# Kernel optimization log

Measured on AMD Instinct MI355X. Metric: run time of the kernel, lower is better.

The kernel has to match this reference:

```python
import jax, jax.numpy as jnp
import numpy as np

HIDDEN = 512
NUM_HEADS = 8
PROJ = NUM_HEADS * HIDDEN  # 4096
B, N = 4, 2048
SCALE = (HIDDEN // NUM_HEADS) ** -0.5  # att_size ** -0.5 = 64 ** -0.5


def setup_inputs() -> dict:
    key = jax.random.key(0)
    ks = jax.random.split(key, 11)
    init = lambda k, shape, fan_in: jax.random.normal(k, shape, jnp.float32) * (fan_in ** -0.5)
    return {
        "q": jax.random.normal(ks[0], (B, N, HIDDEN), jnp.float32),
        "k": jax.random.normal(ks[1], (B, N, HIDDEN), jnp.float32),
        "v": jax.random.normal(ks[2], (B, N, HIDDEN), jnp.float32),
        "Wq": init(ks[3], (HIDDEN, PROJ), HIDDEN),
        "bq": jnp.zeros((PROJ,), jnp.float32),
        "Wk": init(ks[4], (HIDDEN, PROJ), HIDDEN),
        "bk": jnp.zeros((PROJ,), jnp.float32),
        "Wv": init(ks[5], (HIDDEN, PROJ), HIDDEN),
        "bv": jnp.zeros((PROJ,), jnp.float32),
        "Wo": init(ks[6], (PROJ, HIDDEN), PROJ),
        "bo": jnp.zeros((HIDDEN,), jnp.float32),
    }


def reference(q, k, v, Wq, bq, Wk, bk, Wv, bv, Wo, bo):
    # projections expand hidden -> num_heads*hidden (no head splitting in original)
    qp = (q @ Wq + bq) * SCALE          # [B, N, PROJ]
    kp = k @ Wk + bk                    # [B, N, PROJ]
    vp = v @ Wv + bv                    # [B, N, PROJ]
    # bmm(q, k.permute(0,2,1)) -> full [B, Nq, Nk] scores
    scores = jnp.einsum('bnd,bmd->bnm', qp, kp)
    # NON-STANDARD: softmax over dim=1 (the query axis), as in the source
    attn = jax.nn.softmax(scores, axis=1)
    # dropout rate = 0.0 (eval) -> identity
    x = jnp.einsum('bnm,bmd->bnd', attn, vp)  # [B, N, PROJ]
    return x @ Wo + bo                        # [B, N, HIDDEN]
```

## Files before the change

kernel.cpp:

```cpp
#include <hip/hip_runtime.h>
#include <hip/hip_bf16.h>

#define AS1 __attribute__((address_space(1)))
#define AS3 __attribute__((address_space(3)))

typedef __bf16 bf16_t;
typedef __attribute__((ext_vector_type(8))) __bf16 bf16x8;
typedef __attribute__((ext_vector_type(4))) float f32x4;

static constexpr int BSZ = 4, SEQ = 2048, HID = 512, PROJ = 4096;
static constexpr long NROW = (long)BSZ * SEQ;
static constexpr float SCALE = 0.125f;

__device__ __forceinline__ void gload_lds16(const void* g, void* l) {
  __builtin_amdgcn_global_load_lds((const AS1 void*)g, (AS3 void*)l, 16, 0, 0);
}

template <int MAP>
__device__ __forceinline__ long mapk(long c, int s) {
  if (MAP == 0) return c;
  long w = c & ((1L << s) - 1);
  long t = c >> s;
  bool lo = (MAP == 1) ? (t == 1) : (t == 2);
  return (lo ? (1L << s) : 0) + w;
}

__device__ __forceinline__ void stage_half8(
    const bf16_t* __restrict__ G, long ldg, long rcBase, long kcol,
    int half, bf16_t* dst, int tid)
{
#pragma unroll
  for (int it = 0; it < 2; ++it) {
    int li = it * 512 + tid;
    int row = li >> 3;
    int srcb = ((li & 7) << 4) ^ ((row & 7) << 4);
    gload_lds16(G + (rcBase + half * 128 + row) * ldg + kcol + (srcb >> 1),
                (char*)dst + li * 16);
  }
}

#define PH_PRE()  __builtin_amdgcn_s_barrier(); \
                  asm volatile("s_waitcnt lgkmcnt(0)" ::: "memory"); \
                  __builtin_amdgcn_sched_barrier(0); \
                  __builtin_amdgcn_s_setprio(1);
#define PH_POST() __builtin_amdgcn_s_setprio(0); \
                  __builtin_amdgcn_s_barrier(); \
                  __builtin_amdgcn_sched_barrier(0);

__global__ __launch_bounds__(512, 2) void gemm8exp(
    const bf16_t* __restrict__ A, const bf16_t* __restrict__ B,
    bf16_t* __restrict__ C, const float* __restrict__ ra,
    float* __restrict__ part)
{
  constexpr int NT = 24;
  constexpr long LDA = 1024, LDB = 1024;
  constexpr int M = 2048, N = 2048;
  __shared__ __align__(16) bf16_t lds8[65536];

  const int z = blockIdx.z;
  A += (long)z * SEQ * LDA;
  B += (long)z * SEQ * LDB;
  C += (long)z * (long)SEQ * SEQ;

  const int id0 = blockIdx.y * 8 + blockIdx.x;
  const int swz = (id0 & 7) * 8 + (id0 >> 3);
  const int bx = swz & 7, by = swz >> 3;
  const long rowBase = (long)by * 256;
  const long colBase = (long)bx * 256;

  const int tid = threadIdx.x;
  const int lane = tid & 63;
  const int wid = tid >> 6;
  const int wm = wid >> 2;
  const int wn = wid & 3;
  const int l15 = lane & 15;
  const int kgb = (lane >> 4) << 4;

  f32x4 acc[8][4] = {};
  bf16x8 afr[4][2];
  bf16x8 bfr[2][2][2];

  {
    const long ka0 = mapk<1>(0, 9), kb0 = mapk<2>(0, 9);
    const long ka1 = mapk<1>(64, 9);
    stage_half8(A, LDA, rowBase, ka0, 0, lds8 + 0 * 8192, tid);
    stage_half8(A, LDA, rowBase, ka0, 1, lds8 + 1 * 8192, tid);
    stage_half8(B, LDB, colBase, kb0, 0, lds8 + 2 * 8192, tid);
    stage_half8(B, LDB, colBase, kb0, 1, lds8 + 3 * 8192, tid);
    stage_half8(A, LDA, rowBase, ka1, 0, lds8 + 32768 + 0 * 8192, tid);
    asm volatile("s_waitcnt vmcnt(2)" ::: "memory");
    __builtin_amdgcn_s_barrier();
    __builtin_amdgcn_sched_barrier(0);
  }

  for (int t = 0; t < NT; ++t) {
    const int d = t & 1;
    bf16_t* bufc = lds8 + d * 32768;
    bf16_t* bufn = lds8 + (d ^ 1) * 32768;
    const bf16_t* Ah = bufc + wm * 8192;
    const bf16_t* Bh = bufc + 16384 + (wn >> 1) * 8192;
    const long ka1 = mapk<1>((long)(t + 1) * 64, 9);
    const long kb1 = mapk<2>((long)(t + 1) * 64, 9);
    const long ka2 = mapk<1>((long)(t + 2) * 64, 9);

#pragma unroll
    for (int r = 0; r < 4; ++r)
#pragma unroll
      for (int kk = 0; kk < 2; ++kk) {
        int lrow = r * 16 + l15;
        int off = (lrow << 7) + (((kk << 6) + kgb) ^ ((lrow & 7) << 4));
        afr[r][kk] = *(const bf16x8*)((const char*)Ah + off);
      }
#pragma unroll
    for (int c = 0; c < 2; ++c)
#pragma unroll
      for (int kk = 0; kk < 2; ++kk) {
        int lrow = (wn & 1) * 64 + c * 16 + l15;
        int off = (lrow << 7) + (((kk << 6) + kgb) ^ ((lrow & 7) << 4));
        bfr[0][c][kk] = *(const bf16x8*)((const char*)Bh + off);
      }
    if (t + 1 < NT) stage_half8(A, LDA, rowBase, ka1, 1, bufn + 1 * 8192, tid);
    PH_PRE();
#pragma unroll
    for (int r = 0; r < 4; ++r)
#pragma unroll
      for (int c = 0; c < 2; ++c)
#pragma unroll
        for (int kk = 0; kk < 2; ++kk)
          acc[r][c] = __builtin_amdgcn_mfma_f32_16x16x32_bf16(
              afr[r][kk], bfr[0][c][kk], acc[r][c], 0, 0, 0);
    PH_POST();

#pragma unroll
    for (int c = 0; c < 2; ++c)
#pragma unroll
      for (int kk = 0; kk < 2; ++kk) {
        int lrow = (wn & 1) * 64 + 32 + c * 16 + l15;
        int off = (lrow << 7) + (((kk << 6) + kgb) ^ ((lrow & 7) << 4));
        bfr[1][c][kk] = *(const bf16x8*)((const char*)Bh + off);
      }
    if (t + 1 < NT) stage_half8(B, LDB, colBase, kb1, 0, bufn + 2 * 8192, tid);
    PH_PRE();
#pragma unroll
    for (int r = 0; r < 4; ++r)
#pragma unroll
      for (int c = 0; c < 2; ++c)
#pragma unroll
        for (int kk = 0; kk < 2; ++kk)
          acc[r][2 + c] = __builtin_amdgcn_mfma_f32_16x16x32_bf16(
              afr[r][kk], bfr[1][c][kk], acc[r][2 + c], 0, 0, 0);
    PH_POST();

#pragma unroll
    for (int r = 0; r < 4; ++r)
#pragma unroll
      for (int kk = 0; kk < 2; ++kk) {
        int lrow = 64 + r * 16 + l15;
        int off = (lrow << 7) + (((kk << 6) + kgb) ^ ((lrow & 7) << 4));
        afr[r][kk] = *(const bf16x8*)((const char*)Ah + off);
      }
    if (t + 1 < NT) stage_half8(B, LDB, colBase, kb1, 1, bufn + 3 * 8192, tid);
    PH_PRE();
#pragma unroll
    for (int r = 0; r < 4; ++r)
#pragma unroll
      for (int c = 0; c < 2; ++c)
#pragma unroll
        for (int kk = 0; kk < 2; ++kk)
          acc[4 + r][c] = __builtin_amdgcn_mfma_f32_16x16x32_bf16(
              afr[r][kk], bfr[0][c][kk], acc[4 + r][c], 0, 0, 0);
    PH_POST();

    if (t + 2 < NT) stage_half8(A, LDA, rowBase, ka2, 0, bufc + 0 * 8192, tid);
    __builtin_amdgcn_s_barrier();
    __builtin_amdgcn_s_setprio(1);
#pragma unroll
    for (int r = 0; r < 4; ++r)
#pragma unroll
      for (int c = 0; c < 2; ++c)
#pragma unroll
        for (int kk = 0; kk < 2; ++kk)
          acc[4 + r][2 + c] = __builtin_amdgcn_mfma_f32_16x16x32_bf16(
              afr[r][kk], bfr[1][c][kk], acc[4 + r][2 + c], 0, 0, 0);
    __builtin_amdgcn_s_setprio(0);
    if (t < NT - 2) { asm volatile("s_waitcnt vmcnt(2)" ::: "memory"); }
    else            { asm volatile("s_waitcnt vmcnt(0)" ::: "memory"); }
    __builtin_amdgcn_s_barrier();
    __builtin_amdgcn_sched_barrier(0);
  }

  __syncthreads();
  float* cs = (float*)lds8;
  float csum[4] = {0.f, 0.f, 0.f, 0.f};
#pragma unroll
  for (int qr = 0; qr < 2; ++qr)
#pragma unroll
    for (int r = 0; r < 4; ++r) {
      long row0 = rowBase + wm * 128 + qr * 64 + r * 16 + ((lane >> 4) << 2);
      float4 ra4 = *(const float4*)(ra + (long)z * M + row0);
#pragma unroll
      for (int cf = 0; cf < 4; ++cf) {
        long col = colBase + wn * 64 + cf * 16 + l15;
        f32x4 v4 = acc[qr * 4 + r][cf];
        float rr[4] = {ra4.x, ra4.y, ra4.z, ra4.w};
#pragma unroll
        for (int e = 0; e < 4; ++e) {
          float v = __expf(v4[e] + rr[e]);
          C[(row0 + e) * (long)N + col] = (bf16_t)v;
          csum[cf] += v;
        }
      }
    }
#pragma unroll
  for (int cf = 0; cf < 4; ++cf) {
    float s = csum[cf];
    s += __shfl_xor(s, 16);
    s += __shfl_xor(s, 32);
    if (lane < 16) cs[wm * 256 + wn * 64 + cf * 16 + lane] = s;
  }
  __syncthreads();
  if (tid < 256)
    part[((long)by * gridDim.z + z) * N + colBase + tid] = cs[tid] + cs[256 + tid];
}

template <typename OutT, int OUTMODE, int AMAP, int BMAP>
__global__ __launch_bounds__(256) void gemm_bt(
    const bf16_t* __restrict__ A, const bf16_t* __restrict__ B,
    OutT* __restrict__ C, const float* __restrict__ bias,
    float scale, int M, int N, int K, long lda, long ldb,
    long sA, long sB, long sC, long kz, int sshift,
    const bf16_t* __restrict__ A2, const bf16_t* __restrict__ B2,
    OutT* __restrict__ C2, int zSplit)
{
  __shared__ __align__(16) bf16_t As[128 * 64];
  __shared__ __align__(16) bf16_t Bs[128 * 64];
  int z = blockIdx.z;
  if (zSplit > 0 && z >= zSplit) { A = A2; B = B2; C = C2; z -= zSplit; }
  A += (long)z * sA; B += (long)z * sB; C += (long)z * sC;

  const int gx = gridDim.x;
  const int nwg = gx * gridDim.y;
  const int id = blockIdx.y * gx + blockIdx.x;
  const int qq = nwg >> 3, rr = nwg & 7;
  const int xcd = id & 7, jj = id >> 3;
  const int swz = (xcd < rr ? xcd * (qq + 1) : rr * (qq + 1) + (xcd - rr) * qq) + jj;
  const int bx = swz % gx, by = swz / gx;

  const int tid  = threadIdx.x;
  const int lane = tid & 63;
  const int wid  = tid >> 6;
  const int wr = (wid >> 1) * 64;
  const int wc = (wid & 1) * 64;
  const long rowBase = (long)by * 128;
  const long colBase = (long)bx * 128;

  f32x4 acc[4][4] = {};

  int srow[4], scol[4];
#pragma unroll
  for (int i = 0; i < 4; ++i) {
    int li = i * 256 + tid;
    int row = li >> 3;
    int inner = (li & 7) << 4;
    int src = inner ^ ((row & 7) << 4);
    srow[i] = row;
    scol[i] = src >> 1;
  }

  for (int k0 = 0; k0 < K; k0 += 64) {
    const long k0L = kz * z + k0;
    const long ka = mapk<AMAP>(k0L, sshift);
    const long kb = mapk<BMAP>(k0L, sshift);
    __syncthreads();
#pragma unroll
    for (int i = 0; i < 4; ++i) {
      int li = i * 256 + tid;
      gload_lds16(A + (rowBase + srow[i]) * lda + ka + scol[i], (char*)As + li * 16);
      gload_lds16(B + (colBase + srow[i]) * ldb + kb + scol[i], (char*)Bs + li * 16);
    }
    __syncthreads();
#pragma unroll
    for (int kk = 0; kk < 64; kk += 32) {
      const int kbyte = (kk + ((lane >> 4) << 3)) << 1;
      bf16x8 af[4], bfr[4];
#pragma unroll
      for (int m = 0; m < 4; ++m) {
        int row = wr + m * 16 + (lane & 15);
        int off = (row << 7) + (kbyte ^ ((row & 7) << 4));
        af[m] = *(const bf16x8*)((const char*)As + off);
      }
#pragma unroll
      for (int n = 0; n < 4; ++n) {
        int row = wc + n * 16 + (lane & 15);
        int off = (row << 7) + (kbyte ^ ((row & 7) << 4));
        bfr[n] = *(const bf16x8*)((const char*)Bs + off);
      }
#pragma unroll
      for (int m = 0; m < 4; ++m)
#pragma unroll
        for (int n = 0; n < 4; ++n)
          acc[m][n] = __builtin_amdgcn_mfma_f32_16x16x32_bf16(af[m], bfr[n], acc[m][n], 0, 0, 0);
    }
  }

  if (OUTMODE == 2) {
#pragma unroll
    for (int n = 0; n < 4; ++n) {
      const long col = colBase + wc + n * 16 + (lane & 15);
#pragma unroll
      for (int m = 0; m < 4; ++m) {
#pragma unroll
        for (int e = 0; e < 4; ++e) {
          const long row = rowBase + wr + m * 16 + (lane >> 4) * 4 + e;
          float v = acc[m][n][e] * scale;
          bf16_t h = (bf16_t)v;
          bf16_t l = (bf16_t)(v - (float)h);
          C[row * (2L * N) + col] = (OutT)h;
          C[row * (2L * N) + N + col] = (OutT)l;
        }
      }
    }
  } else {
#pragma unroll
    for (int n = 0; n < 4; ++n) {
      const long col = colBase + wc + n * 16 + (lane & 15);
      const float bv_ = bias ? bias[col] : 0.0f;
#pragma unroll
      for (int m = 0; m < 4; ++m) {
#pragma unroll
        for (int e = 0; e < 4; ++e) {
          const long row = rowBase + wr + m * 16 + (lane >> 4) * 4 + e;
          C[row * (long)N + col] = (OutT)((acc[m][n][e] + bv_) * scale);
        }
      }
    }
  }
}

__global__ void split2_b3(const float* __restrict__ in0, const float* __restrict__ in1,
                          const float* __restrict__ in2,
                          bf16_t* __restrict__ o0, bf16_t* __restrict__ o1,
                          bf16_t* __restrict__ o2, long n, int cshift) {
  const float* in = (blockIdx.y == 0) ? in0 : (blockIdx.y == 1) ? in1 : in2;
  bf16_t* out = (blockIdx.y == 0) ? o0 : (blockIdx.y == 1) ? o1 : o2;
  long C = 1L << cshift;
  long i0 = ((long)blockIdx.x * blockDim.x + threadIdx.x) * 4;
  long stride = (long)gridDim.x * blockDim.x * 4;
  for (long i = i0; i < n; i += stride) {
    float4 f = *(const float4*)(in + i);
    long r = i >> cshift, c = i & (C - 1);
    union { ushort4 u; bf16_t h[4]; } H, L;
    float fv[4] = {f.x, f.y, f.z, f.w};
#pragma unroll
    for (int j = 0; j < 4; ++j) {
      bf16_t h = (bf16_t)fv[j];
      H.h[j] = h;
      L.h[j] = (bf16_t)(fv[j] - (float)h);
    }
    *(ushort4*)(out + r * 2 * C + c) = H.u;
    *(ushort4*)(out + r * 2 * C + C + c) = L.u;
  }
}

__global__ void transpose_split2(const float* __restrict__ in, bf16_t* __restrict__ out,
                                 int R, int C) {
  __shared__ float tile[32][33];
  int c0 = blockIdx.x * 32, r0 = blockIdx.y * 32;
  int tx = threadIdx.x & 31, ty = threadIdx.x >> 5;
#pragma unroll
  for (int i = 0; i < 32; i += 8)
    tile[ty + i][tx] = in[(long)(r0 + ty + i) * C + (c0 + tx)];
  __syncthreads();
#pragma unroll
  for (int i = 0; i < 32; i += 8) {
    float x = tile[tx][ty + i];
    bf16_t h = (bf16_t)x;
    bf16_t l = (bf16_t)(x - (float)h);
    long o = (long)(c0 + ty + i) * 2 * R + (r0 + tx);
    out[o] = h;
    out[o + R] = l;
  }
}

__global__ void cast_f32_bf16(const float* __restrict__ in, bf16_t* __restrict__ out, long n) {
  long i0 = ((long)blockIdx.x * blockDim.x + threadIdx.x) * 4;
  long stride = (long)gridDim.x * blockDim.x * 4;
  for (long i = i0; i < n; i += stride) {
    float4 f = *(const float4*)(in + i);
    union { ushort4 u; bf16_t h[4]; } o;
    o.h[0] = (bf16_t)f.x; o.h[1] = (bf16_t)f.y; o.h[2] = (bf16_t)f.z; o.h[3] = (bf16_t)f.w;
    *(ushort4*)(out + i) = o.u;
  }
}

__global__ void reduce2(const float* __restrict__ gp, const float* __restrict__ wp,
                        bf16_t* __restrict__ Gtcat, bf16_t* __restrict__ WvoTb,
                        float scale, int nElem, int nParts) {
  int i = blockIdx.x * 256 + threadIdx.x;
  if (i < nElem) {
    float a = 0.f, b = 0.f;
    for (int p = 0; p < nParts; ++p) {
      a += gp[(long)p * nElem + i];
      b += wp[(long)p * nElem + i];
    }
    a *= scale;
    int r = i >> 9, c = i & 511;
    bf16_t h = (bf16_t)a;
    Gtcat[(long)r * 1024 + c] = h;
    Gtcat[(long)r * 1024 + 512 + c] = (bf16_t)(a - (float)h);
    WvoTb[i] = (bf16_t)b;
  }
}

__global__ void rank1(const float* __restrict__ Wq, const float* __restrict__ bk,
                      const float* __restrict__ bq,
                      const bf16_t* __restrict__ WoS, const float* __restrict__ bv,
                      float* __restrict__ wqbk, float* __restrict__ bvo,
                      float* __restrict__ cdot) {
  __shared__ float red[256];
  int y = blockIdx.y, bx = blockIdx.x, t = threadIdx.x;
  float s = 0.f;
  if (y == 0) {
    for (int j = t; j < PROJ; j += 256) s += Wq[(long)bx * PROJ + j] * bk[j];
  } else if (y == 1) {
    const bf16_t* row = WoS + (long)bx * 2 * PROJ;
    for (int j = t; j < PROJ; j += 256)
      s += ((float)row[j] + (float)row[PROJ + j]) * bv[j];
  } else {
    if (bx != 0) return;
    for (int j = t; j < PROJ; j += 256) s += bq[j] * bk[j];
  }
  red[t] = s; __syncthreads();
  for (int w = 128; w > 0; w >>= 1) {
    if (t < w) red[t] += red[t + w];
    __syncthreads();
  }
  if (t == 0) {
    if (y == 0) wqbk[bx] = red[0];
    else if (y == 1) bvo[bx] = red[0];
    else *cdot = red[0];
  }
}

__global__ void rowdot_rav(const float* __restrict__ q, const float* __restrict__ wqbk,
                           const float* __restrict__ cdot, float* __restrict__ rav) {
  __shared__ float red[256];
  int r = blockIdx.x, t = threadIdx.x;
  float s = 0.f;
  for (int j = t; j < HID; j += 256) s += q[(long)r * HID + j] * wqbk[j];
  red[t] = s; __syncthreads();
  for (int w = 128; w > 0; w >>= 1) {
    if (t < w) red[t] += red[t + w];
    __syncthreads();
  }
  if (t == 0) rav[r] = SCALE * (red[0] + *cdot);
}

__global__ void colsum_final(const float* __restrict__ part, float* __restrict__ crcp,
                             int Nm, int nParts) {
  int b = blockIdx.y;
  int m = blockIdx.x * 256 + threadIdx.x;
  float s = 0.f;
  for (int p = 0; p < nParts; ++p)
    s += part[((long)p * gridDim.y + b) * Nm + m];
  crcp[(long)b * Nm + m] = 1.0f / s;
}

__device__ __forceinline__ float bf2f(unsigned short u) {
  union { unsigned u32; float f; } x; x.u32 = ((unsigned)u) << 16; return x.f;
}

__global__ void transpose_scale_bf16(const bf16_t* __restrict__ in, const float* __restrict__ crcp,
                                     bf16_t* __restrict__ out, int R, int C, long sIn, long sOut) {
  __shared__ bf16_t tile[64][68];
  int z = blockIdx.z;
  const bf16_t* ip = in + (long)z * sIn;
  bf16_t* op = out + (long)z * sOut;
  const float* rc = crcp + (long)z * R;
  int c0 = blockIdx.x * 64, r0 = blockIdx.y * 64;
#pragma unroll
  for (int i = 0; i < 4; ++i) {
    int chunk = i * 256 + threadIdx.x;
    int r = chunk >> 4, c4 = (chunk & 15) << 2;
    float s = rc[r0 + r];
    ushort4 uv = *(const ushort4*)(ip + (long)(r0 + r) * C + (c0 + c4));
    tile[r][c4 + 0] = (bf16_t)(bf2f(uv.x) * s);
    tile[r][c4 + 1] = (bf16_t)(bf2f(uv.y) * s);
    tile[r][c4 + 2] = (bf16_t)(bf2f(uv.z) * s);
    tile[r][c4 + 3] = (bf16_t)(bf2f(uv.w) * s);
  }
  __syncthreads();
#pragma unroll
  for (int i = 0; i < 4; ++i) {
    int chunk = i * 256 + threadIdx.x;
    int oc = chunk >> 4, or4 = (chunk & 15) << 2;
    union { ushort4 u; bf16_t h[4]; } o;
    o.h[0] = tile[or4 + 0][oc];
    o.h[1] = tile[or4 + 1][oc];
    o.h[2] = tile[or4 + 2][oc];
    o.h[3] = tile[or4 + 3][oc];
    *(ushort4*)(op + (long)(c0 + oc) * R + (r0 + or4)) = o.u;
  }
}

extern "C" void kernel_launch(void* const* d_in, const int* in_sizes, int n_in,
                              void* d_out, int out_size, void* d_ws, size_t ws_size,
                              hipStream_t stream)
{
  (void)in_sizes; (void)n_in; (void)out_size; (void)ws_size;
  const float* q  = (const float*)d_in[0];
  const float* k  = (const float*)d_in[1];
  const float* v  = (const float*)d_in[2];
  const float* Wq = (const float*)d_in[3];
  const float* bq = (const float*)d_in[4];
  const float* Wk = (const float*)d_in[5];
  const float* bk = (const float*)d_in[6];
  const float* Wv = (const float*)d_in[7];
  const float* bv = (const float*)d_in[8];
  const float* Wo = (const float*)d_in[9];
  const float* bo = (const float*)d_in[10];
  float* out = (float*)d_out;

  char* ws = (char*)d_ws;
  const size_t MB = 1u << 20;
  bf16_t* qcat  = (bf16_t*)(ws);
  bf16_t* kcat  = (bf16_t*)(ws + 16 * MB);
  bf16_t* GA    = (bf16_t*)(ws + 32 * MB);
  bf16_t* GB    = (bf16_t*)(ws + 40 * MB);
  bf16_t* WoS   = (bf16_t*)(ws + 48 * MB);
  bf16_t* WvS   = (bf16_t*)(ws + 56 * MB);
  float*  Gpart = (float*)(ws + 64 * MB);
  float*  WvoTp = (float*)(ws + 80 * MB);
  bf16_t* Gtcat = (bf16_t*)(ws + 97 * MB);
  bf16_t* WvoTb = (bf16_t*)(ws + 98 * MB);
  float*  bvo   = (float*)(ws + 99 * MB);
  float*  wqbk  = (float*)(ws + 99 * MB + 16 * 1024);
  float*  cdot  = (float*)(ws + 99 * MB + 48 * 1024);
  float*  rav   = (float*)(ws + 99 * MB + 64 * 1024);
  float*  crcp  = (float*)(ws + 99 * MB + 192 * 1024);
  float*  part  = (float*)(ws + 99 * MB + 256 * 1024);
  bf16_t* tcat  = (bf16_t*)(ws + 100 * MB);
  bf16_t* vbf   = (bf16_t*)(ws + 116 * MB);
  bf16_t* vo    = (bf16_t*)(ws + 124 * MB);
  bf16_t* vosT  = (bf16_t*)(ws + 132 * MB);
  bf16_t* P     = (bf16_t*)(ws + 140 * MB);

  split2_b3<<<dim3(1024, 2), 256, 0, stream>>>(q, k, nullptr, qcat, kcat, nullptr,
      NROW * HID, 9);
  split2_b3<<<dim3(1024, 3), 256, 0, stream>>>(Wk, Wq, Wv, GA, GB, WvS,
      (long)HID * PROJ, 12);
  transpose_split2<<<dim3(HID / 32, PROJ / 32), 256, 0, stream>>>(Wo, WoS, PROJ, HID);

  gemm_bt<float, 0, 1, 2><<<dim3(4, 4, 32), 256, 0, stream>>>(GA, GB, Gpart,
      nullptr, 1.0f, HID, HID, 768, 2L * PROJ, 2L * PROJ,
      0, 0, (long)HID * HID, 768, 12, WoS, WvS, WvoTp, 16);
  reduce2<<<(HID * HID + 255) / 256, 256, 0, stream>>>(Gpart, WvoTp, Gtcat, WvoTb,
      SCALE, HID * HID, 16);

  rank1<<<dim3(HID, 3), 256, 0, stream>>>(Wq, bk, bq, WoS, bv, wqbk, bvo, cdot);
  rowdot_rav<<<(int)NROW, 256, 0, stream>>>(q, wqbk, cdot, rav);

  gemm_bt<bf16_t, 2, 1, 2><<<dim3(4, 64, 1), 256, 0, stream>>>(qcat, Gtcat, tcat,
      nullptr, 1.0f, (int)NROW, HID, 1536, 1024, 1024, 0, 0, 0, 0, 9,
      nullptr, nullptr, nullptr, 0);

  cast_f32_bf16<<<2048, 256, 0, stream>>>(v, vbf, NROW * HID);

  gemm8exp<<<dim3(8, 8, BSZ), 512, 0, stream>>>(tcat, kcat, P, rav, part);
  colsum_final<<<dim3(SEQ / 256, BSZ), 256, 0, stream>>>(part, crcp, SEQ, 8);

  gemm_bt<bf16_t, 0, 0, 0><<<dim3(4, 64, 1), 256, 0, stream>>>(vbf, WvoTb, vo,
      bvo, 1.0f, (int)NROW, HID, HID, HID, HID, 0, 0, 0, 0, 0,
      nullptr, nullptr, nullptr, 0);
  transpose_scale_bf16<<<dim3(HID / 64, SEQ / 64, BSZ), 256, 0, stream>>>(
      vo, crcp, vosT, SEQ, HID, (long)SEQ * HID, (long)HID * SEQ);

  gemm_bt<float, 0, 0, 0><<<dim3(4, 16, BSZ), 256, 0, stream>>>(P, vosT, out,
      bo, 1.0f, SEQ, HID, SEQ, SEQ, SEQ,
      (long)SEQ * SEQ, (long)HID * SEQ, (long)SEQ * HID, 0, 0,
      nullptr, nullptr, nullptr, 0);
}
```

Baseline: 232.4 us.

## Merge v cast and vo GEMM into existing launches, trim Wvo split-K

The float-to-bf16 cast of v moves into the q/k split kernel as a third y-slice that writes only the hi part. The vbf×WvoTb GEMM is batched into the same launch as the qcat×Gtcat GEMM through a z-split, with per-half K, strides, bias and output mode. This requires turning the output mode from a template parameter into a runtime argument. The Wvo weight-fold GEMM now uses 6 split-K partitions instead of 16, dropping most of the lo-part correction terms. Together these cut kernel launches and weight-prep work, at the cost of a runtime branch in the GEMM epilogue and lower precision in the folded Wvo weights.

```diff
diff --git a/kernel.cpp b/kernel.cpp
--- a/kernel.cpp
+++ b/kernel.cpp
@@ -223,19 +223,24 @@
     part[((long)by * gridDim.z + z) * N + colBase + tid] = cs[tid] + cs[256 + tid];
 }
 
-template <typename OutT, int OUTMODE, int AMAP, int BMAP>
+template <typename OutT, int AMAP, int BMAP>
 __global__ __launch_bounds__(256) void gemm_bt(
     const bf16_t* __restrict__ A, const bf16_t* __restrict__ B,
     OutT* __restrict__ C, const float* __restrict__ bias,
     float scale, int M, int N, int K, long lda, long ldb,
-    long sA, long sB, long sC, long kz, int sshift,
+    long sA, long sB, long sC, long kz, int sshift, int outm,
     const bf16_t* __restrict__ A2, const bf16_t* __restrict__ B2,
-    OutT* __restrict__ C2, int zSplit)
+    OutT* __restrict__ C2, const float* __restrict__ bias2,
+    int K2, long lda2, long ldb2, int outm2, int zSplit)
 {
   __shared__ __align__(16) bf16_t As[128 * 64];
   __shared__ __align__(16) bf16_t Bs[128 * 64];
   int z = blockIdx.z;
-  if (zSplit > 0 && z >= zSplit) { A = A2; B = B2; C = C2; z -= zSplit; }
+  if (zSplit > 0 && z >= zSplit) {
+    A = A2; B = B2; C = C2; bias = bias2;
+    K = K2; lda = lda2; ldb = ldb2; outm = outm2;
+    z -= zSplit;
+  }
   A += (long)z * sA; B += (long)z * sB; C += (long)z * sC;
 
   const int gx = gridDim.x;
@@ -303,7 +308,7 @@
     }
   }
 
-  if (OUTMODE == 2) {
+  if (outm == 2) {
 #pragma unroll
     for (int n = 0; n < 4; ++n) {
       const long col = colBase + wc + n * 16 + (lane & 15);
@@ -340,15 +345,15 @@
 __global__ void split2_b3(const float* __restrict__ in0, const float* __restrict__ in1,
                           const float* __restrict__ in2,
                           bf16_t* __restrict__ o0, bf16_t* __restrict__ o1,
-                          bf16_t* __restrict__ o2, long n, int cshift) {
+                          bf16_t* __restrict__ o2, long n, int cshift, int castMask) {
   const float* in = (blockIdx.y == 0) ? in0 : (blockIdx.y == 1) ? in1 : in2;
   bf16_t* out = (blockIdx.y == 0) ? o0 : (blockIdx.y == 1) ? o1 : o2;
+  const bool castOnly = (castMask >> blockIdx.y) & 1;
   long C = 1L << cshift;
   long i0 = ((long)blockIdx.x * blockDim.x + threadIdx.x) * 4;
   long stride = (long)gridDim.x * blockDim.x * 4;
   for (long i = i0; i < n; i += stride) {
     float4 f = *(const float4*)(in + i);
-    long r = i >> cshift, c = i & (C - 1);
     union { ushort4 u; bf16_t h[4]; } H, L;
     float fv[4] = {f.x, f.y, f.z, f.w};
 #pragma unroll
@@ -357,8 +362,13 @@
       H.h[j] = h;
       L.h[j] = (bf16_t)(fv[j] - (float)h);
     }
-    *(ushort4*)(out + r * 2 * C + c) = H.u;
-    *(ushort4*)(out + r * 2 * C + C + c) = L.u;
+    if (castOnly) {
+      *(ushort4*)(out + i) = H.u;
+    } else {
+      long r = i >> cshift, c = i & (C - 1);
+      *(ushort4*)(out + r * 2 * C + c) = H.u;
+      *(ushort4*)(out + r * 2 * C + C + c) = L.u;
+    }
   }
 }
 
@@ -382,27 +392,14 @@
   }
 }
 
-__global__ void cast_f32_bf16(const float* __restrict__ in, bf16_t* __restrict__ out, long n) {
-  long i0 = ((long)blockIdx.x * blockDim.x + threadIdx.x) * 4;
-  long stride = (long)gridDim.x * blockDim.x * 4;
-  for (long i = i0; i < n; i += stride) {
-    float4 f = *(const float4*)(in + i);
-    union { ushort4 u; bf16_t h[4]; } o;
-    o.h[0] = (bf16_t)f.x; o.h[1] = (bf16_t)f.y; o.h[2] = (bf16_t)f.z; o.h[3] = (bf16_t)f.w;
-    *(ushort4*)(out + i) = o.u;
-  }
-}
-
 __global__ void reduce2(const float* __restrict__ gp, const float* __restrict__ wp,
                         bf16_t* __restrict__ Gtcat, bf16_t* __restrict__ WvoTb,
-                        float scale, int nElem, int nParts) {
+                        float scale, int nElem, int nP1, int nP2) {
   int i = blockIdx.x * 256 + threadIdx.x;
   if (i < nElem) {
     float a = 0.f, b = 0.f;
-    for (int p = 0; p < nParts; ++p) {
-      a += gp[(long)p * nElem + i];
-      b += wp[(long)p * nElem + i];
-    }
+    for (int p = 0; p < nP1; ++p) a += gp[(long)p * nElem + i];
+    for (int p = 0; p < nP2; ++p) b += wp[(long)p * nElem + i];
     a *= scale;
     int r = i >> 9, c = i & 511;
     bf16_t h = (bf16_t)a;
@@ -545,38 +542,34 @@
   bf16_t* vosT  = (bf16_t*)(ws + 132 * MB);
   bf16_t* P     = (bf16_t*)(ws + 140 * MB);
 
-  split2_b3<<<dim3(1024, 2), 256, 0, stream>>>(q, k, nullptr, qcat, kcat, nullptr,
-      NROW * HID, 9);
+  split2_b3<<<dim3(1024, 3), 256, 0, stream>>>(q, k, v, qcat, kcat, vbf,
+      NROW * HID, 9, 0b100);
   split2_b3<<<dim3(1024, 3), 256, 0, stream>>>(Wk, Wq, Wv, GA, GB, WvS,
-      (long)HID * PROJ, 12);
+      (long)HID * PROJ, 12, 0);
   transpose_split2<<<dim3(HID / 32, PROJ / 32), 256, 0, stream>>>(Wo, WoS, PROJ, HID);
 
-  gemm_bt<float, 0, 1, 2><<<dim3(4, 4, 32), 256, 0, stream>>>(GA, GB, Gpart,
+  gemm_bt<float, 1, 2><<<dim3(4, 4, 22), 256, 0, stream>>>(GA, GB, Gpart,
       nullptr, 1.0f, HID, HID, 768, 2L * PROJ, 2L * PROJ,
-      0, 0, (long)HID * HID, 768, 12, WoS, WvS, WvoTp, 16);
+      0, 0, (long)HID * HID, 768, 12, 0,
+      WoS, WvS, WvoTp, nullptr, 768, 2L * PROJ, 2L * PROJ, 0, 16);
   reduce2<<<(HID * HID + 255) / 256, 256, 0, stream>>>(Gpart, WvoTp, Gtcat, WvoTb,
-      SCALE, HID * HID, 16);
+      SCALE, HID * HID, 16, 6);
 
   rank1<<<dim3(HID, 3), 256, 0, stream>>>(Wq, bk, bq, WoS, bv, wqbk, bvo, cdot);
   rowdot_rav<<<(int)NROW, 256, 0, stream>>>(q, wqbk, cdot, rav);
 
-  gemm_bt<bf16_t, 2, 1, 2><<<dim3(4, 64, 1), 256, 0, stream>>>(qcat, Gtcat, tcat,
-      nullptr, 1.0f, (int)NROW, HID, 1536, 1024, 1024, 0, 0, 0, 0, 9,
-      nullptr, nullptr, nullptr, 0);
-
-  cast_f32_bf16<<<2048, 256, 0, stream>>>(v, vbf, NROW * HID);
+  gemm_bt<bf16_t, 1, 2><<<dim3(4, 64, 2), 256, 0, stream>>>(qcat, Gtcat, tcat,
+      nullptr, 1.0f, (int)NROW, HID, 1536, 1024, 1024, 0, 0, 0, 0, 9, 2,
+      vbf, WvoTb, vo, bvo, HID, HID, HID, 0, 1);
 
   gemm8exp<<<dim3(8, 8, BSZ), 512, 0, stream>>>(tcat, kcat, P, rav, part);
   colsum_final<<<dim3(SEQ / 256, BSZ), 256, 0, stream>>>(part, crcp, SEQ, 8);
 
-  gemm_bt<bf16_t, 0, 0, 0><<<dim3(4, 64, 1), 256, 0, stream>>>(vbf, WvoTb, vo,
-      bvo, 1.0f, (int)NROW, HID, HID, HID, HID, 0, 0, 0, 0, 0,
-      nullptr, nullptr, nullptr, 0);
   transpose_scale_bf16<<<dim3(HID / 64, SEQ / 64, BSZ), 256, 0, stream>>>(
       vo, crcp, vosT, SEQ, HID, (long)SEQ * HID, (long)HID * SEQ);
 
-  gemm_bt<float, 0, 0, 0><<<dim3(4, 16, BSZ), 256, 0, stream>>>(P, vosT, out,
+  gemm_bt<float, 0, 0><<<dim3(4, 16, BSZ), 256, 0, stream>>>(P, vosT, out,
       bo, 1.0f, SEQ, HID, SEQ, SEQ, SEQ,
-      (long)SEQ * SEQ, (long)HID * SEQ, (long)SEQ * HID, 0, 0,
-      nullptr, nullptr, nullptr, 0);
-}
+      (long)SEQ * SEQ, (long)HID * SEQ, (long)SEQ * HID, 0, 0, 0,
+      nullptr, nullptr, nullptr, nullptr, 0, 0, 0, 0, 0);
+}
```

Result: faster. 210.2 us (-9.6%).
